# Performance work log

Measured on AMD Instinct MI355X. Metric: run time of the kernel, lower is better.

Reference implementation:

```python
import jax, jax.numpy as jnp
import numpy as np


def setup_inputs() -> dict:
    key = jax.random.key(0)
    k = jax.random.split(key, 6)
    BS, T, ZCH, H, W = 16, 8, 256, 16, 16
    VOCAB, EMB = 4096, 256
    x = jax.random.uniform(k[0], (BS, T, ZCH, H, W), dtype=jnp.float32)
    # Embedding init mirrors uniform_(-1/vocab, 1/vocab)
    codebook = jax.random.uniform(k[1], (VOCAB, EMB), dtype=jnp.float32,
                                  minval=-1.0 / VOCAB, maxval=1.0 / VOCAB)
    pre_w = jax.random.normal(k[2], (EMB, ZCH), dtype=jnp.float32) * 0.02
    pre_b = jax.random.normal(k[3], (EMB,), dtype=jnp.float32) * 0.02
    post_w = jax.random.normal(k[4], (ZCH, EMB), dtype=jnp.float32) * 0.02
    post_b = jax.random.normal(k[5], (ZCH,), dtype=jnp.float32) * 0.02
    return {"x": x, "codebook": codebook, "pre_w": pre_w, "pre_b": pre_b,
            "post_w": post_w, "post_b": post_b}


def reference(x, codebook, pre_w, pre_b, post_w, post_b):
    bs, t, zch, h, w = x.shape
    vocab, emb = codebook.shape
    # preprocess: [0,1] -> [-1,1]
    xp = x * 2.0 - 1.0
    # flatten time into batch; encoder is identity (external module)
    z_in = xp.reshape(bs * t, zch, h, w)
    # pre_quantize_conv: 1x1 conv == per-pixel linear (z_ch -> emb)
    z = jnp.einsum('bchw,ec->behw', z_in, pre_w) + pre_b[None, :, None, None]
    # flatten: (b h w) e  -- matches rearrange('b e h w -> (b h w) e')
    zf = z.transpose(0, 2, 3, 1).reshape(-1, emb)  # [N, emb]
    # squared cdist via expansion: ||z||^2 + ||c||^2 - 2 z.c
    z_sq = jnp.sum(zf * zf, axis=-1, keepdims=True)          # [N,1]
    c_sq = jnp.sum(codebook * codebook, axis=-1)             # [V]
    dist = z_sq + c_sq[None, :] - 2.0 * (zf @ codebook.T)    # [N,V]
    tokens = jnp.argmin(dist, axis=-1)                        # [N]
    zq = codebook[tokens]                                     # [N, emb] gather
    zq = zq.reshape(bs * t, h, w, emb).transpose(0, 3, 1, 2)  # b e h w
    # straight-through estimator
    dec_in = z + jax.lax.stop_gradient(zq - z)
    # post_quantize_conv: 1x1 conv (emb -> z_ch); decoder is identity
    recon = jnp.einsum('behw,ce->bchw', dec_in, post_w) + post_b[None, :, None, None]
    z_out = z.reshape(bs, t, emb, h, w)
    zq_out = zq.reshape(bs, t, emb, h, w)
    recon_out = recon.reshape(bs, t, zch, h, w)
    tokens_out = tokens.reshape(bs, t, h * w)
    return z_out, zq_out, recon_out, tokens_out
```

## Files before the change

kernel.cpp:

```cpp
#include <hip/hip_runtime.h>
#include <float.h>
#include <stdint.h>

#define BB   128
#define CCH  256
#define EMB_ 256
#define HW   256
#define NPIX 32768
#define VOC  4096

typedef _Float16 f16x8 __attribute__((ext_vector_type(8)));
typedef float    f32x4 __attribute__((ext_vector_type(4)));

__device__ __forceinline__ void async16(void* lds, const void* g) {
    __builtin_amdgcn_global_load_lds((const __attribute__((address_space(1))) uint32_t*)g,
                                     (__attribute__((address_space(3))) uint32_t*)lds,
                                     16, 0, 0);
}

__global__ __launch_bounds__(256) void k_prep(const float* __restrict__ cb,
                                              const float* __restrict__ post_w,
                                              const float* __restrict__ post_b,
                                              const float* __restrict__ pre_w,
                                              float* __restrict__ postcode,
                                              _Float16* __restrict__ B3,
                                              float* __restrict__ csq,
                                              _Float16* __restrict__ W3) {
    __shared__ float smem[4352];
    const int bid = blockIdx.x;
    const int tid = threadIdx.x;

    if (bid < 256) {
        float (*cbs)[EMB_] = (float(*)[EMB_])smem;
        int v0 = bid * 16;
        int c  = tid;
#pragma unroll
        for (int r = 0; r < 16; ++r)
            cbs[r][c] = cb[(v0 + r) * EMB_ + c];
        __syncthreads();
        float acc[16];
        float bias = post_b[c];
#pragma unroll
        for (int r = 0; r < 16; ++r) acc[r] = bias;
        const float4* w4p = (const float4*)(post_w + c * EMB_);
        for (int e4 = 0; e4 < 64; ++e4) {
            float4 w4 = w4p[e4];
#pragma unroll
            for (int r = 0; r < 16; ++r) {
                float4 c4 = *(const float4*)&cbs[r][e4 * 4];
                acc[r] = fmaf(w4.x, c4.x, fmaf(w4.y, c4.y,
                         fmaf(w4.z, c4.z, fmaf(w4.w, c4.w, acc[r]))));
            }
        }
#pragma unroll
        for (int r = 0; r < 16; ++r)
            postcode[(v0 + r) * CCH + c] = acc[r];
    } else if (bid < 512) {
        float (*cs)[17] = (float(*)[17])smem;
        int vg = bid - 256;
        int vr = tid >> 4, e0 = (tid & 15) << 4;
        const float* cp = cb + (vg * 16 + vr) * EMB_ + e0;
#pragma unroll
        for (int j = 0; j < 16; ++j)
            cs[e0 + j][vr] = cp[j];
        __syncthreads();
#pragma unroll
        for (int it = 0; it < 4; ++it) {
            int c = it * 256 + tid;
            int kc8 = c >> 4, row = c & 15;
            int lo = kc8 >> 5;
            int kh = kc8 & 31;
            f16x8 outv;
#pragma unroll
            for (int j = 0; j < 8; ++j) {
                float v = cs[kh * 8 + j][row] * 65536.0f;
                _Float16 h = (_Float16)v;
                if (lo) h = (_Float16)(v - (float)h);
                outv[j] = h;
            }
            *(f16x8*)(B3 + ((vg * 64 + kc8) * 128 + row * 8)) = outv;
        }
    } else if (bid < 528) {
        int v = (bid - 512) * 256 + tid;
        const float4* row = (const float4*)(cb + v * EMB_);
        float s = 0.f;
#pragma unroll 8
        for (int q = 0; q < 64; ++q) {
            float4 a = row[q];
            s = fmaf(a.x, a.x, fmaf(a.y, a.y, fmaf(a.z, a.z, fmaf(a.w, a.w, s))));
        }
        csq[v] = s;
    } else {
        int eg = bid - 528;
#pragma unroll
        for (int i = 0; i < 4; ++i) {
            int flat = i * 256 + tid;
            int u = flat >> 4, row = flat & 15;
            int part = u >> 5, c8 = u & 31;
            const float* wp = pre_w + (eg * 16 + row) * CCH + c8 * 8;
            f16x8 outv;
#pragma unroll
            for (int j = 0; j < 8; ++j) {
                float v = wp[j] * 16.0f;
                _Float16 h = (_Float16)v;
                if (part) h = (_Float16)((v - (float)h) * 4096.0f);
                outv[j] = h;
            }
            *(f16x8*)(W3 + ((eg * 64 + u) * 128 + row * 8)) = outv;
        }
    }
}

__global__ __launch_bounds__(512) void k_zgemm(const float* __restrict__ x,
                                               const _Float16* __restrict__ W3,
                                               const float* __restrict__ pre_b,
                                               float* __restrict__ zout,
                                               _Float16* __restrict__ A3) {
    __shared__ __align__(16) char smem[99328];
    float* pbs = (float*)(smem + 98304);

    const int tid = threadIdx.x;
    const int l   = tid & 63;
    const int w   = tid >> 6;
    const int l15 = l & 15, l4 = l >> 4;
    const int wr  = w >> 2, wc = w & 3;
    const int bM  = blockIdx.x;
    const int b   = bM >> 1, hw0 = (bM & 1) * 128;

    const int xng = tid >> 6, xu = (tid >> 4) & 3, xrow = tid & 15;
    const float* xbase = x + (size_t)b * (CCH * HW) + hw0 + xng * 16 + xrow;

#define STAGE_W(CC, BUF) {                                                   \
    _Pragma("unroll")                                                        \
    for (int i = 0; i < 2; ++i) {                                            \
        int flat = i * 512 + tid; int eg = flat >> 6, sub = flat & 63;       \
        async16((_Float16*)(smem + (BUF) * 16384) + flat * 8,                \
                W3 + (eg * 64 + (CC) * 4) * 128 + sub * 8);                  \
        async16((_Float16*)(smem + 32768 + (BUF) * 16384) + flat * 8,        \
                W3 + (eg * 64 + 32 + (CC) * 4) * 128 + sub * 8);             \
    } }

#define STAGE_X(CC, BUF) {                                                   \
    const float* xp_ = xbase + ((CC) * 32 + xu * 8) * HW;                    \
    f16x8 hv, lv;                                                            \
    _Pragma("unroll")                                                        \
    for (int j = 0; j < 8; ++j) {                                            \
        float xv = 2.0f * xp_[j * HW] - 1.0f;                     \
        _Float16 h = (_Float16)xv;                                           \
        lv[j] = (_Float16)((xv - (float)h) * 4096.0f);   \
        hv[j] = h;                                                           \
    }                                                                        \
    *(f16x8*)((_Float16*)(smem + 65536 + (BUF) * 8192) + tid * 8) = hv;      \
    *(f16x8*)((_Float16*)(smem + 81920 + (BUF) * 8192) + tid * 8) = lv;      \
    }

    if (tid < 256) pbs[tid] = pre_b[tid];
    STAGE_W(0, 0)
    STAGE_X(0, 0)
    __syncthreads();

    f32x4 accA[4][4], accB[4][4];
    const f32x4 zero4 = {0.f, 0.f, 0.f, 0.f};
#pragma unroll
    for (int m = 0; m < 4; ++m)
#pragma unroll
        for (int s = 0; s < 4; ++s) { accA[m][s] = zero4; accB[m][s] = zero4; }

    int buf = 0;
    for (int cc = 0; cc < 8; ++cc) {
        if (cc < 7) { STAGE_W(cc + 1, buf ^ 1) STAGE_X(cc + 1, buf ^ 1) }
        const _Float16* WhC = (const _Float16*)(smem + buf * 16384);
        const _Float16* WlC = (const _Float16*)(smem + 32768 + buf * 16384);
        const _Float16* XhC = (const _Float16*)(smem + 65536 + buf * 8192);
        const _Float16* XlC = (const _Float16*)(smem + 81920 + buf * 8192);
        f16x8 whf[4], wlf[4], xhf[4], xlf[4];
#pragma unroll
        for (int m = 0; m < 4; ++m) {
            whf[m] = *(const f16x8*)&WhC[((wc * 4 + m) * 64 + l4 * 16 + l15) * 8];
            wlf[m] = *(const f16x8*)&WlC[((wc * 4 + m) * 64 + l4 * 16 + l15) * 8];
        }
#pragma unroll
        for (int s = 0; s < 4; ++s) {
            xhf[s] = *(const f16x8*)&XhC[((wr * 4 + s) * 64 + l4 * 16 + l15) * 8];
            xlf[s] = *(const f16x8*)&XlC[((wr * 4 + s) * 64 + l4 * 16 + l15) * 8];
        }
#pragma unroll
        for (int m = 0; m < 4; ++m)
#pragma unroll
            for (int s = 0; s < 4; ++s)
                accA[m][s] = __builtin_amdgcn_mfma_f32_16x16x32_f16(whf[m], xhf[s], accA[m][s], 0, 0, 0);
#pragma unroll
        for (int m = 0; m < 4; ++m)
#pragma unroll
            for (int s = 0; s < 4; ++s)
                accB[m][s] = __builtin_amdgcn_mfma_f32_16x16x32_f16(whf[m], xlf[s], accB[m][s], 0, 0, 0);
#pragma unroll
        for (int m = 0; m < 4; ++m)
#pragma unroll
            for (int s = 0; s < 4; ++s)
                accB[m][s] = __builtin_amdgcn_mfma_f32_16x16x32_f16(wlf[m], xhf[s], accB[m][s], 0, 0, 0);
        __syncthreads();
        buf ^= 1;
    }

    float* zw = (float*)(smem + w * 5120);
    const size_t zbase = (size_t)b * (EMB_ * HW) + hw0;
#pragma unroll
    for (int m = 0; m < 4; ++m) {
        asm volatile("s_waitcnt lgkmcnt(0)" ::: "memory");
        __builtin_amdgcn_sched_barrier(0);
        f32x4 zv[4];
#pragma unroll
        for (int s = 0; s < 4; ++s) {
#pragma unroll
            for (int r = 0; r < 4; ++r) {
                float g = fmaf(accB[m][s][r], 0x1p-12f, accA[m][s][r]) * 0x1p-4f;
                zv[s][r] = g + pbs[wc * 64 + m * 16 + l4 * 4 + r];
            }
            *(f32x4*)(zw + (s * 16 + l15) * 20 + l4 * 4) = zv[s];
#pragma unroll
            for (int r = 0; r < 4; ++r)
                zout[zbase + (size_t)(wc * 64 + m * 16 + l4 * 4 + r) * HW
                     + wr * 64 + s * 16 + l15] = zv[s][r];
        }
        asm volatile("s_waitcnt lgkmcnt(0)" ::: "memory");
        __builtin_amdgcn_sched_barrier(0);
#pragma unroll
        for (int o = 0; o < 4; ++o) {
            int flat = o * 64 + l;
            int part = flat >> 7, rest = flat & 127;
            int pg = rest >> 5, uq = (rest >> 4) & 1, row = rest & 15;
            int nloc = pg * 16 + row;
            float4 va = *(const float4*)(zw + nloc * 20 + uq * 8);
            float4 vb = *(const float4*)(zw + nloc * 20 + uq * 8 + 4);
            float vs[8] = {va.x, va.y, va.z, va.w, vb.x, vb.y, vb.z, vb.w};
            f16x8 outv;
#pragma unroll
            for (int j = 0; j < 8; ++j) {
                float v = vs[j] * 256.0f;
                _Float16 h = (_Float16)v;
                if (part) h = (_Float16)(v - (float)h);
                outv[j] = h;
            }
            *(f16x8*)(A3 + ((size_t)(bM * 8 + wr * 4 + pg) * 64
                            + part * 32 + wc * 8 + m * 2 + uq) * 128 + row * 8) = outv;
        }
    }
#undef STAGE_W
#undef STAGE_X
}

__device__ __forceinline__ void issueA(const _Float16* __restrict__ A3, int bM,
                                       int w, int l, _Float16* dst, int kA) {
#pragma unroll
    for (int i = 0; i < 2; ++i) {
        int pg = 2 * w + i;
        const _Float16* g = A3 + ((bM * 16 + pg) * 64 + kA) * 128 + l * 8;
        async16(dst + pg * 512, g);
    }
}

__device__ __forceinline__ void issueB(const _Float16* __restrict__ B3, int vgbase,
                                       int w, int l, _Float16* dst, int kB) {
#pragma unroll
    for (int i = 0; i < 2; ++i) {
        int vg = 2 * w + i;
        const _Float16* g = B3 + ((vgbase + vg) * 64 + kB) * 128 + l * 8;
        async16(dst + vg * 512, g);
    }
}

__global__ __launch_bounds__(512) void k_dist(const float* __restrict__ zout,
                                              const _Float16* __restrict__ A3,
                                              const _Float16* __restrict__ B3,
                                              const float* __restrict__ csq,
                                              float* __restrict__ bestw,
                                              int* __restrict__ bidxw) {
    __shared__ __align__(16) _Float16 Ab[3][8192];
    __shared__ __align__(16) _Float16 Bb[3][8192];
    __shared__ float csq_s[2048];
    __shared__ float zsq_s[256];
    __shared__ float red_b[8][128];
    __shared__ int   red_i[8][128];

    const int tid = threadIdx.x;
    const int l   = tid & 63;
    const int w   = tid >> 6;
    const int l15 = l & 15, l4 = l >> 4;
    const int wr  = w >> 2, wc = w & 3;
    const int bM  = blockIdx.x & 127;
    const int nh  = blockIdx.x >> 7;
    const int vgb = nh * 128;

    issueA(A3, bM, w, l, Ab[0], 0);
    issueB(B3, vgb, w, l, Bb[0], 0);
    issueA(A3, bM, w, l, Ab[1], 4);
    issueB(B3, vgb, w, l, Bb[1], 4);

#pragma unroll
    for (int j = 0; j < 4; ++j) csq_s[j * 512 + tid] = csq[nh * 2048 + j * 512 + tid];

    if (tid < 256) {
        const float* zp = zout + bM * (EMB_ * HW) + tid;
        float s = 0.f;
        for (int k = 0; k < 256; ++k) { float zv = zp[k * HW]; s = fmaf(zv, zv, s); }
        zsq_s[tid] = s;
    }
    __syncthreads();

    float best[32]; int bidx[32];
#pragma unroll
    for (int i = 0; i < 32; ++i) { best[i] = FLT_MAX; bidx[i] = 0; }

    const f32x4 zero4 = {0.f, 0.f, 0.f, 0.f};
    int cur = 0;
    for (int vt = 0; vt < 8; ++vt) {
        f32x4 acc[8][4];
#pragma unroll
        for (int s = 0; s < 8; ++s)
#pragma unroll
            for (int m = 0; m < 4; ++m) acc[s][m] = zero4;

        for (int kc = 0; kc < 24; ++kc) {
            const int n = vt * 24 + kc;
            int kc2 = kc + 2, vt2 = vt;
            if (kc2 >= 24) { kc2 -= 24; ++vt2; }
            const int nxt = (cur + 2 >= 3) ? cur - 1 : cur + 2;
            const bool pf = (vt2 < 8);
            const int kA2 = ((kc2 >= 16) ? 32 : 0) + (kc2 & 7) * 4;
            const int kB2 = ((kc2 >= 8 && kc2 < 16) ? 32 : 0) + (kc2 & 7) * 4;

            f16x8 af0[4], bf[4];
#pragma unroll
            for (int s = 0; s < 4; ++s)
                af0[s] = *(const f16x8*)&Ab[cur][(wr * 8 + s) * 512 + l4 * 128 + l15 * 8];
#pragma unroll
            for (int m = 0; m < 4; ++m)
                bf[m] = *(const f16x8*)&Bb[cur][(wc * 4 + m) * 512 + l4 * 128 + l15 * 8];
            if (pf) issueA(A3, bM, w, l, Ab[nxt], kA2);
            __builtin_amdgcn_s_barrier();
            asm volatile("s_waitcnt lgkmcnt(0)" ::: "memory");
            __builtin_amdgcn_sched_barrier(0);
            __builtin_amdgcn_s_setprio(1);
#pragma unroll
            for (int s = 0; s < 4; ++s)
#pragma unroll
                for (int m = 0; m < 4; ++m)
                    acc[s][m] = __builtin_amdgcn_mfma_f32_16x16x32_f16(af0[s], bf[m], acc[s][m], 0, 0, 0);
            __builtin_amdgcn_s_setprio(0);
            __builtin_amdgcn_s_barrier();

            f16x8 af1[4];
#pragma unroll
            for (int s = 0; s < 4; ++s)
                af1[s] = *(const f16x8*)&Ab[cur][(wr * 8 + 4 + s) * 512 + l4 * 128 + l15 * 8];
            if (pf) issueB(B3, vgb + vt2 * 16, w, l, Bb[nxt], kB2);
            __builtin_amdgcn_s_barrier();
            asm volatile("s_waitcnt lgkmcnt(0)" ::: "memory");
            __builtin_amdgcn_sched_barrier(0);
            __builtin_amdgcn_s_setprio(1);
#pragma unroll
            for (int s = 0; s < 4; ++s)
#pragma unroll
                for (int m = 0; m < 4; ++m)
                    acc[4 + s][m] = __builtin_amdgcn_mfma_f32_16x16x32_f16(af1[s], bf[m], acc[4 + s][m], 0, 0, 0);
            __builtin_amdgcn_s_setprio(0);
            if (n == 190) { asm volatile("s_waitcnt vmcnt(0)" ::: "memory"); }
            else          { asm volatile("s_waitcnt vmcnt(4)" ::: "memory"); }
            __builtin_amdgcn_s_barrier();
            __builtin_amdgcn_sched_barrier(0);
            cur = (cur + 1 >= 3) ? 0 : cur + 1;
        }

#pragma unroll
        for (int m = 0; m < 4; ++m) {
            int cl = vt * 256 + (wc * 4 + m) * 16 + l15;
            float cs = csq_s[cl];
            int code = nh * 2048 + cl;
#pragma unroll
            for (int s = 0; s < 8; ++s)
#pragma unroll
                for (int r = 0; r < 4; ++r) {
                    float dd = (zsq_s[wr * 128 + s * 16 + l4 * 4 + r] + cs)
                               - acc[s][m][r] * 0x1p-23f;
                    int pi = s * 4 + r;
                    if (dd < best[pi]) { best[pi] = dd; bidx[pi] = code; }
                }
        }
    }

#pragma unroll
    for (int off = 8; off >= 1; off >>= 1) {
#pragma unroll
        for (int i = 0; i < 32; ++i) {
            float ob = __shfl_xor(best[i], off, 64);
            int   oi = __shfl_xor(bidx[i], off, 64);
            if (ob < best[i] || (ob == best[i] && oi < bidx[i])) { best[i] = ob; bidx[i] = oi; }
        }
    }
    if (l15 == 0) {
#pragma unroll
        for (int s = 0; s < 8; ++s)
#pragma unroll
            for (int r = 0; r < 4; ++r) {
                int pl = s * 16 + l4 * 4 + r;
                red_b[w][pl] = best[s * 4 + r];
                red_i[w][pl] = bidx[s * 4 + r];
            }
    }
    __syncthreads();
    if (tid < 256) {
        int wrg = tid >> 7, pl = tid & 127;
        float bb = red_b[wrg * 4][pl]; int bi = red_i[wrg * 4][pl];
#pragma unroll
        for (int c = 1; c < 4; ++c) {
            float ob = red_b[wrg * 4 + c][pl]; int oi = red_i[wrg * 4 + c][pl];
            if (ob < bb || (ob == bb && oi < bi)) { bb = ob; bi = oi; }
        }
        bestw[nh * NPIX + bM * 256 + tid] = bb;
        bidxw[nh * NPIX + bM * 256 + tid] = bi;
    }
}

__global__ __launch_bounds__(256) void k_argmin2(const float* __restrict__ bestw,
                                                 const int* __restrict__ bidxw,
                                                 float* __restrict__ tok_f) {
    int i = blockIdx.x * 256 + threadIdx.x;
    float b0 = bestw[i], b1 = bestw[NPIX + i];
    int   i0 = bidxw[i], i1 = bidxw[NPIX + i];
    tok_f[i] = (float)((b1 < b0) ? i1 : i0);
}

__global__ __launch_bounds__(256) void k_gather(const float* __restrict__ tok_f,
                                                const float* __restrict__ cb,
                                                const float* __restrict__ postcode,
                                                float* __restrict__ zq_out,
                                                float* __restrict__ recon) {
    int b  = blockIdx.x >> 3;
    int e0 = (blockIdx.x & 7) * 32;
    int hw = threadIdx.x;
    int t  = (int)tok_f[b * HW + hw];
    const float* cbr = cb       + t * EMB_;
    const float* pcr = postcode + t * CCH;
    float* zq = zq_out + b * (EMB_ * HW) + hw;
    float* rc = recon  + b * (CCH * HW) + hw;
#pragma unroll
    for (int j = 0; j < 32; ++j) {
        int e = e0 + j;
        zq[e * HW] = cbr[e];
        rc[e * HW] = pcr[e];
    }
}

__global__ __launch_bounds__(256) void k_gather2(const float* __restrict__ bestw,
                                                 const int* __restrict__ bidxw,
                                                 const float* __restrict__ cb,
                                                 const float* __restrict__ postcode,
                                                 float* __restrict__ zq_out,
                                                 float* __restrict__ recon,
                                                 float* __restrict__ tok_f) {
    __shared__ float rows[64][257];
    __shared__ int   toks[64];
    const int b    = blockIdx.x >> 1;
    const int half = blockIdx.x & 1;
    const int tid  = threadIdx.x;
    const int p    = tid & 63, eg = tid >> 6;

    for (int g = 0; g < 2; ++g) {
        int px0 = half * 128 + g * 64;
        if (tid < 64) {
            int i = b * HW + px0 + tid;
            float b0 = bestw[i], b1 = bestw[NPIX + i];
            int   i0 = bidxw[i], i1 = bidxw[NPIX + i];
            int t = (b1 < b0) ? i1 : i0;
            toks[tid] = t;
            tok_f[i] = (float)t;
        }
        __syncthreads();
#pragma unroll 8
        for (int r = 0; r < 64; ++r)
            rows[r][tid] = cb[(size_t)toks[r] * EMB_ + tid];
        __syncthreads();
        {
            float* zq = zq_out + (size_t)b * (EMB_ * HW) + px0 + p;
#pragma unroll 8
            for (int eo = 0; eo < 64; ++eo) {
                int e = eg * 64 + eo;
                zq[(size_t)e * HW] = rows[p][e];
            }
        }
        __syncthreads();
#pragma unroll 8
        for (int r = 0; r < 64; ++r)
            rows[r][tid] = postcode[(size_t)toks[r] * CCH + tid];
        __syncthreads();
        {
            float* rc = recon + (size_t)b * (CCH * HW) + px0 + p;
#pragma unroll 8
            for (int eo = 0; eo < 64; ++eo) {
                int e = eg * 64 + eo;
                rc[(size_t)e * HW] = rows[p][e];
            }
        }
        __syncthreads();
    }
}

extern "C" void kernel_launch(void* const* d_in, const int* in_sizes, int n_in,
                              void* d_out, int out_size, void* d_ws, size_t ws_size,
                              hipStream_t stream) {
    const float* x      = (const float*)d_in[0];
    const float* cb     = (const float*)d_in[1];
    const float* pre_w  = (const float*)d_in[2];
    const float* pre_b  = (const float*)d_in[3];
    const float* post_w = (const float*)d_in[4];
    const float* post_b = (const float*)d_in[5];

    float* out    = (float*)d_out;
    float* z_out  = out;
    float* zq_out = out + 8388608;
    float* recon  = out + 16777216;
    float* tok_f  = out + 25165824;

    _Float16* A3 = (_Float16*)zq_out;
    _Float16* B3 = (_Float16*)recon;
    _Float16* W3 = (_Float16*)(recon + 1048576 + 4 * NPIX);

    float* csq      = (float*)d_ws;
    float* postcode = csq + VOC;

    size_t need = (size_t)(VOC + VOC * CCH + 4 * NPIX) * sizeof(float);
    bool fused = (ws_size >= need);
    float* bestw; int* bidxw;
    if (fused) {
        bestw = postcode + (size_t)VOC * CCH;
        bidxw = (int*)(bestw + 2 * NPIX);
    } else {
        bestw = recon + 1048576;
        bidxw = (int*)(recon + 1048576 + 2 * NPIX);
    }

    k_prep <<< 544, 256, 0, stream>>>(cb, post_w, post_b, pre_w,
                                      postcode, B3, csq, W3);
    k_zgemm<<< 256, 512, 0, stream>>>(x, W3, pre_b, z_out, A3);
    k_dist <<< 256, 512, 0, stream>>>(z_out, A3, B3, csq, bestw, bidxw);
    if (fused) {
        k_gather2<<< 256, 256, 0, stream>>>(bestw, bidxw, cb, postcode,
                                            zq_out, recon, tok_f);
    } else {
        k_argmin2<<< 128, 256, 0, stream>>>(bestw, bidxw, tok_f);
        k_gather <<<1024, 256, 0, stream>>>(tok_f, cb, postcode, zq_out, recon);
    }
}
```

Measured before the change: 390.0 us.

## Halve zgemm pixel tile, read weights from global, shrink LDS for occupancy

k_zgemm now processes 64 pixels per block instead of 128, doubling the grid to 512 blocks. Weight fragments are loaded straight from global memory (through cache) instead of being staged in LDS, and pre_b is kept in registers. This cuts LDS use from about 97KB to 36KB and adds a launch-bounds occupancy hint, so more blocks fit per CU and the many CUs are better filled. The cost is redundant global weight reads across blocks and only half the threads doing the x staging.

Result: slower. 401.9 us (+3.0%).

```diff
diff --git a/kernel.cpp b/kernel.cpp
--- a/kernel.cpp
+++ b/kernel.cpp
@@ -111,126 +111,123 @@
     }
 }
 
-__global__ __launch_bounds__(512) void k_zgemm(const float* __restrict__ x,
-                                               const _Float16* __restrict__ W3,
-                                               const float* __restrict__ pre_b,
-                                               float* __restrict__ zout,
-                                               _Float16* __restrict__ A3) {
-    __shared__ __align__(16) char smem[99328];
-    float* pbs = (float*)(smem + 98304);
+__global__ __launch_bounds__(512, 4) void k_zgemm(const float* __restrict__ x,
+                                                  const _Float16* __restrict__ W3,
+                                                  const float* __restrict__ pre_b,
+                                                  float* __restrict__ zout,
+                                                  _Float16* __restrict__ A3) {
+    __shared__ __align__(16) char smem[36864];
 
     const int tid = threadIdx.x;
     const int l   = tid & 63;
     const int w   = tid >> 6;
     const int l15 = l & 15, l4 = l >> 4;
     const int wr  = w >> 2, wc = w & 3;
-    const int bM  = blockIdx.x;
-    const int b   = bM >> 1, hw0 = (bM & 1) * 128;
+    const int bQ  = blockIdx.x;
+    const int b   = bQ >> 2, hw0 = (bQ & 3) * 64;
 
     const int xng = tid >> 6, xu = (tid >> 4) & 3, xrow = tid & 15;
     const float* xbase = x + (size_t)b * (CCH * HW) + hw0 + xng * 16 + xrow;
 
-#define STAGE_W(CC, BUF) {                                                   \
-    _Pragma("unroll")                                                        \
-    for (int i = 0; i < 2; ++i) {                                            \
-        int flat = i * 512 + tid; int eg = flat >> 6, sub = flat & 63;       \
-        async16((_Float16*)(smem + (BUF) * 16384) + flat * 8,                \
-                W3 + (eg * 64 + (CC) * 4) * 128 + sub * 8);                  \
-        async16((_Float16*)(smem + 32768 + (BUF) * 16384) + flat * 8,        \
-                W3 + (eg * 64 + 32 + (CC) * 4) * 128 + sub * 8);             \
+#define STAGE_X(CC, BUF) {                                                   \
+    if (tid < 256) {                                                         \
+        const float* xp_ = xbase + ((CC) * 32 + xu * 8) * HW;                \
+        f16x8 hv, lv;                                                        \
+        _Pragma("unroll")                                                    \
+        for (int j = 0; j < 8; ++j) {                                        \
+            float xv = 2.0f * xp_[j * HW] - 1.0f;                 \
+            _Float16 h = (_Float16)xv;                                       \
+            lv[j] = (_Float16)((xv - (float)h) * 4096.0f);   \
+            hv[j] = h;                                                       \
+        }                                                                    \
+        int slot = ((xng * 4 + xu) * 16 + xrow) * 8;                         \
+        *(f16x8*)((_Float16*)(smem + (BUF) * 4096) + slot) = hv;             \
+        *(f16x8*)((_Float16*)(smem + 8192 + (BUF) * 4096) + slot) = lv;      \
     } }
 
-#define STAGE_X(CC, BUF) {                                                   \
-    const float* xp_ = xbase + ((CC) * 32 + xu * 8) * HW;                    \
-    f16x8 hv, lv;                                                            \
-    _Pragma("unroll")                                                        \
-    for (int j = 0; j < 8; ++j) {                                            \
-        float xv = 2.0f * xp_[j * HW] - 1.0f;                     \
-        _Float16 h = (_Float16)xv;                                           \
-        lv[j] = (_Float16)((xv - (float)h) * 4096.0f);   \
-        hv[j] = h;                                                           \
-    }                                                                        \
-    *(f16x8*)((_Float16*)(smem + 65536 + (BUF) * 8192) + tid * 8) = hv;      \
-    *(f16x8*)((_Float16*)(smem + 81920 + (BUF) * 8192) + tid * 8) = lv;      \
-    }
-
-    if (tid < 256) pbs[tid] = pre_b[tid];
-    STAGE_W(0, 0)
+    float4 pb4[4];
+#pragma unroll
+    for (int m = 0; m < 4; ++m)
+        pb4[m] = *(const float4*)&pre_b[wc * 64 + m * 16 + l4 * 4];
+
     STAGE_X(0, 0)
     __syncthreads();
 
-    f32x4 accA[4][4], accB[4][4];
+    const _Float16* wbase[4];
+#pragma unroll
+    for (int m = 0; m < 4; ++m)
+        wbase[m] = W3 + ((size_t)(wc * 4 + m) * 64 + l4) * 128 + l15 * 8;
+
+    f32x4 accA[4][2], accB[4][2];
     const f32x4 zero4 = {0.f, 0.f, 0.f, 0.f};
 #pragma unroll
     for (int m = 0; m < 4; ++m)
 #pragma unroll
-        for (int s = 0; s < 4; ++s) { accA[m][s] = zero4; accB[m][s] = zero4; }
+        for (int s = 0; s < 2; ++s) { accA[m][s] = zero4; accB[m][s] = zero4; }
 
     int buf = 0;
     for (int cc = 0; cc < 8; ++cc) {
-        if (cc < 7) { STAGE_W(cc + 1, buf ^ 1) STAGE_X(cc + 1, buf ^ 1) }
-        const _Float16* WhC = (const _Float16*)(smem + buf * 16384);
-        const _Float16* WlC = (const _Float16*)(smem + 32768 + buf * 16384);
-        const _Float16* XhC = (const _Float16*)(smem + 65536 + buf * 8192);
-        const _Float16* XlC = (const _Float16*)(smem + 81920 + buf * 8192);
-        f16x8 whf[4], wlf[4], xhf[4], xlf[4];
+        if (cc < 7) STAGE_X(cc + 1, buf ^ 1)
+        f16x8 whf[4], wlf[4];
 #pragma unroll
         for (int m = 0; m < 4; ++m) {
-            whf[m] = *(const f16x8*)&WhC[((wc * 4 + m) * 64 + l4 * 16 + l15) * 8];
-            wlf[m] = *(const f16x8*)&WlC[((wc * 4 + m) * 64 + l4 * 16 + l15) * 8];
-        }
-#pragma unroll
-        for (int s = 0; s < 4; ++s) {
-            xhf[s] = *(const f16x8*)&XhC[((wr * 4 + s) * 64 + l4 * 16 + l15) * 8];
-            xlf[s] = *(const f16x8*)&XlC[((wr * 4 + s) * 64 + l4 * 16 + l15) * 8];
+            whf[m] = *(const f16x8*)(wbase[m] + (size_t)cc * 512);
+            wlf[m] = *(const f16x8*)(wbase[m] + (size_t)cc * 512 + 4096);
+        }
+        f16x8 xhf[2], xlf[2];
+#pragma unroll
+        for (int s = 0; s < 2; ++s) {
+            int xoff = (((wr * 2 + s) * 4 + l4) * 16 + l15) * 8;
+            xhf[s] = *(const f16x8*)((_Float16*)(smem + buf * 4096) + xoff);
+            xlf[s] = *(const f16x8*)((_Float16*)(smem + 8192 + buf * 4096) + xoff);
         }
 #pragma unroll
         for (int m = 0; m < 4; ++m)
 #pragma unroll
-            for (int s = 0; s < 4; ++s)
+            for (int s = 0; s < 2; ++s)
                 accA[m][s] = __builtin_amdgcn_mfma_f32_16x16x32_f16(whf[m], xhf[s], accA[m][s], 0, 0, 0);
 #pragma unroll
         for (int m = 0; m < 4; ++m)
 #pragma unroll
-            for (int s = 0; s < 4; ++s)
+            for (int s = 0; s < 2; ++s)
                 accB[m][s] = __builtin_amdgcn_mfma_f32_16x16x32_f16(whf[m], xlf[s], accB[m][s], 0, 0, 0);
 #pragma unroll
         for (int m = 0; m < 4; ++m)
 #pragma unroll
-            for (int s = 0; s < 4; ++s)
+            for (int s = 0; s < 2; ++s)
                 accB[m][s] = __builtin_amdgcn_mfma_f32_16x16x32_f16(wlf[m], xhf[s], accB[m][s], 0, 0, 0);
         __syncthreads();
         buf ^= 1;
     }
 
-    float* zw = (float*)(smem + w * 5120);
+    float* zw = (float*)(smem + 16384 + w * 2560);
     const size_t zbase = (size_t)b * (EMB_ * HW) + hw0;
 #pragma unroll
     for (int m = 0; m < 4; ++m) {
         asm volatile("s_waitcnt lgkmcnt(0)" ::: "memory");
         __builtin_amdgcn_sched_barrier(0);
-        f32x4 zv[4];
-#pragma unroll
-        for (int s = 0; s < 4; ++s) {
+        f32x4 zv[2];
+#pragma unroll
+        for (int s = 0; s < 2; ++s) {
 #pragma unroll
             for (int r = 0; r < 4; ++r) {
                 float g = fmaf(accB[m][s][r], 0x1p-12f, accA[m][s][r]) * 0x1p-4f;
-                zv[s][r] = g + pbs[wc * 64 + m * 16 + l4 * 4 + r];
+                zv[s][r] = g + pb4[m][r];
             }
             *(f32x4*)(zw + (s * 16 + l15) * 20 + l4 * 4) = zv[s];
 #pragma unroll
             for (int r = 0; r < 4; ++r)
                 zout[zbase + (size_t)(wc * 64 + m * 16 + l4 * 4 + r) * HW
-                     + wr * 64 + s * 16 + l15] = zv[s][r];
+                     + wr * 32 + s * 16 + l15] = zv[s][r];
         }
         asm volatile("s_waitcnt lgkmcnt(0)" ::: "memory");
         __builtin_amdgcn_sched_barrier(0);
 #pragma unroll
-        for (int o = 0; o < 4; ++o) {
+        for (int o = 0; o < 2; ++o) {
             int flat = o * 64 + l;
-            int part = flat >> 7, rest = flat & 127;
-            int pg = rest >> 5, uq = (rest >> 4) & 1, row = rest & 15;
-            int nloc = pg * 16 + row;
+            int part = flat >> 6, rest = flat & 63;
+            int pg2 = rest >> 5, uq = (rest >> 4) & 1, row = rest & 15;
+            int nloc = pg2 * 16 + row;
             float4 va = *(const float4*)(zw + nloc * 20 + uq * 8);
             float4 vb = *(const float4*)(zw + nloc * 20 + uq * 8 + 4);
             float vs[8] = {va.x, va.y, va.z, va.w, vb.x, vb.y, vb.z, vb.w};
@@ -242,11 +239,11 @@
                 if (part) h = (_Float16)(v - (float)h);
                 outv[j] = h;
             }
-            *(f16x8*)(A3 + ((size_t)(bM * 8 + wr * 4 + pg) * 64
+            int pixg = b * 16 + (bQ & 3) * 4 + wr * 2 + pg2;
+            *(f16x8*)(A3 + ((size_t)pixg * 64
                             + part * 32 + wc * 8 + m * 2 + uq) * 128 + row * 8) = outv;
         }
     }
-#undef STAGE_W
 #undef STAGE_X
 }
 
@@ -542,7 +539,7 @@
 
     k_prep <<< 544, 256, 0, stream>>>(cb, post_w, post_b, pre_w,
                                       postcode, B3, csq, W3);
-    k_zgemm<<< 256, 512, 0, stream>>>(x, W3, pre_b, z_out, A3);
+    k_zgemm<<< 512, 512, 0, stream>>>(x, W3, pre_b, z_out, A3);
     k_dist <<< 256, 512, 0, stream>>>(z_out, A3, B3, csq, bestw, bidxw);
     if (fused) {
         k_gather2<<< 256, 256, 0, stream>>>(bestw, bidxw, cb, postcode,
```
